# Kernel optimization log

Measured on AMD Instinct MI355X. Metric: run time of the kernel, lower is better.

Reference implementation:

```python
import jax, jax.numpy as jnp
import numpy as np

B, SRC_LEN, IN_DIM = 4096, 128, 16
H = 64
SEQ_LEN = 100
MEAN_DIM = 4
COV_DIM = MEAN_DIM + MEAN_DIM * (MEAN_DIM - 1) // 2  # 10
SKIP = 4


def _lin_init(key, out_d, in_d):
    k1, k2 = jax.random.split(key)
    bound = 1.0 / np.sqrt(in_d)
    W = jax.random.uniform(k1, (out_d, in_d), minval=-bound, maxval=bound, dtype=jnp.float32)
    b = jax.random.uniform(k2, (out_d,), minval=-bound, maxval=bound, dtype=jnp.float32)
    return W, b


def setup_inputs() -> dict:
    key = jax.random.key(0)
    ks = jax.random.split(key, 16)
    inp = {}
    inp["x"] = jax.random.normal(ks[0], (B, SRC_LEN, IN_DIM), dtype=jnp.float32)
    inp["trg"] = jax.random.normal(ks[1], (B, 1, SKIP), dtype=jnp.float32)
    # encoder GRU (1 layer)
    inp["enc_Wih"], inp["enc_bih"] = _lin_init(ks[2], 3 * H, IN_DIM)
    inp["enc_Whh"], inp["enc_bhh"] = _lin_init(ks[3], 3 * H, H)
    # decoder GRU (1 layer)
    inp["dec_Wih"], inp["dec_bih"] = _lin_init(ks[4], 3 * H, IN_DIM)
    inp["dec_Whh"], inp["dec_bhh"] = _lin_init(ks[5], 3 * H, H)
    # decoder.out: Linear(H -> IN_DIM)
    inp["out_W"], inp["out_b"] = _lin_init(ks[6], IN_DIM, H)
    # initEmbed: Linear(SKIP -> IN_DIM)
    inp["emb_W"], inp["emb_b"] = _lin_init(ks[7], IN_DIM, SKIP)
    # mean head: Linear(IN_DIM->H), GELU, Linear(H->MEAN_DIM)
    inp["mh_W1"], inp["mh_b1"] = _lin_init(ks[8], H, IN_DIM)
    inp["mh_W2"], inp["mh_b2"] = _lin_init(ks[9], MEAN_DIM, H)
    # cov head: Linear(IN_DIM->H), GELU, Linear(H->COV_DIM)
    inp["ch_W1"], inp["ch_b1"] = _lin_init(ks[10], H, IN_DIM)
    inp["ch_W2"], inp["ch_b2"] = _lin_init(ks[11], COV_DIM, H)
    return inp


def _gru_cell(h, xt, Wih, Whh, bih, bhh):
    # PyTorch GRU cell math. h, xt: [B, H], [B, in]
    gi = xt @ Wih.T + bih           # [B, 3H]
    gh = h @ Whh.T + bhh            # [B, 3H]
    i_r, i_z, i_n = jnp.split(gi, 3, axis=-1)
    h_r, h_z, h_n = jnp.split(gh, 3, axis=-1)
    r = jax.nn.sigmoid(i_r + h_r)
    z = jax.nn.sigmoid(i_z + h_z)
    n = jnp.tanh(i_n + r * h_n)
    return (1.0 - z) * n + z * h


def reference(x, trg, enc_Wih, enc_bih, enc_Whh, enc_bhh,
              dec_Wih, dec_bih, dec_Whh, dec_bhh,
              out_W, out_b, emb_W, emb_b,
              mh_W1, mh_b1, mh_W2, mh_b2,
              ch_W1, ch_b1, ch_W2, ch_b2):
    b = x.shape[0]
    # ---- encoder GRU over src_len; only final hidden is used downstream ----
    h0 = jnp.zeros((b, H), dtype=x.dtype)

    def enc_step(h, xt):
        h = _gru_cell(h, xt, enc_Wih, enc_Whh, enc_bih, enc_bhh)
        return h, None

    enc_h, _ = jax.lax.scan(enc_step, h0, jnp.swapaxes(x, 0, 1))

    init_in = trg[:, 0, :] @ emb_W.T + emb_b  # [B, IN_DIM]

    def dec_step(carry, _):
        h, inp = carry
        h = _gru_cell(h, inp, dec_Wih, dec_Whh, dec_bih, dec_bhh)
        o = h @ out_W.T + out_b               # [B, IN_DIM]
        nxt = jax.lax.stop_gradient(o)        # .detach() on fed-back input
        return (h, nxt), o

    (_, _), outs = jax.lax.scan(dec_step, (enc_h, init_in), None, length=SEQ_LEN)
    dec_out = jnp.swapaxes(outs, 0, 1)        # [B, SEQ_LEN, IN_DIM]

    # ---- output heads (Dropout is identity in eval) ----
    means = jax.nn.gelu(dec_out @ mh_W1.T + mh_b1, approximate=False) @ mh_W2.T + mh_b2
    covs = jax.nn.gelu(dec_out @ ch_W1.T + ch_b1, approximate=False) @ ch_W2.T + ch_b2

    inf = jnp.inf
    lower = jnp.array([-inf, -inf, -1.0, -1.0], dtype=means.dtype)
    upper = jnp.array([inf, inf, 1.0, 1.0], dtype=means.dtype)
    means = jnp.maximum(jnp.minimum(means, upper), lower)
    return means, covs
```

## Files before the change

kernel.cpp:

```cpp
#include <hip/hip_runtime.h>
#include <cstdint>
#include <cstddef>

#define BTOT    4096
#define SRCLEN  128
#define INDIM   16
#define HDIM    64
#define SEQLEN  100
#define MEANS_N (BTOT * SEQLEN * 4)

__device__ __forceinline__ float sigmoidf_(float x) { return 1.0f / (1.0f + __expf(-x)); }
__device__ __forceinline__ float tanhf_(float x) {
    float e = __expf(2.0f * x);
    return 1.0f - 2.0f / (e + 1.0f);
}
__device__ __forceinline__ float gelu_exact(float x) {
    return 0.5f * x * (1.0f + erff(x * 0.70710678118654752440f));
}

typedef __attribute__((ext_vector_type(8))) short s8v;
typedef __attribute__((ext_vector_type(4))) float f4v;

__device__ __forceinline__ unsigned short f2bf(float x) {
    unsigned u = __float_as_uint(x);
    unsigned r = (u + 0x7FFFu + ((u >> 16) & 1u)) >> 16;
    return (unsigned short)r;
}
__device__ __forceinline__ float bf2f(unsigned short b) {
    return __uint_as_float(((unsigned)b) << 16);
}
__device__ __forceinline__ void split2(float4 a, float4 b, s8v& hi, s8v& lo) {
    float v[8] = {a.x, a.y, a.z, a.w, b.x, b.y, b.z, b.w};
    #pragma unroll
    for (int j = 0; j < 8; ++j) {
        unsigned short h = f2bf(v[j]);
        hi[j] = (short)h;
        lo[j] = (short)f2bf(v[j] - bf2f(h));
    }
}
__device__ __forceinline__ void split8(const float* v, s8v& hi, s8v& lo) {
    #pragma unroll
    for (int j = 0; j < 8; ++j) {
        unsigned short h = f2bf(v[j]);
        hi[j] = (short)h;
        lo[j] = (short)f2bf(v[j] - bf2f(h));
    }
}
__device__ __forceinline__ void load_bfrag(const float* p, s8v& hi, s8v& lo) {
    float4 a = *(const float4*)p;
    float4 b = *(const float4*)(p + 4);
    split2(a, b, hi, lo);
}

#define MFMA16(a, b, c) __builtin_amdgcn_mfma_f32_16x16x32_bf16((a), (b), (c), 0, 0, 0)

__global__ __launch_bounds__(256, 1) void enc_mfma_kernel(
    const float* __restrict__ x,
    const float* __restrict__ Wih, const float* __restrict__ bih,
    const float* __restrict__ Whh, const float* __restrict__ bhh,
    float* __restrict__ enc_h)
{
    const int tid  = threadIdx.x;
    const int lane = tid & 63;
    const int w    = tid >> 6;
    const int col  = lane & 15;
    const int q    = lane >> 4;
    const int u    = w * 16 + col;
    const int b0   = blockIdx.x * 16;

    __shared__ __align__(16) unsigned short hiL[2][16][72];
    __shared__ __align__(16) unsigned short loL[2][16][72];

    for (int i = tid; i < 16 * 72; i += 256) {
        ((unsigned short*)hiL)[i] = 0;
        ((unsigned short*)loL)[i] = 0;
    }

    const s8v z8 = {0, 0, 0, 0, 0, 0, 0, 0};
    const f4v z4 = {0.0f, 0.0f, 0.0f, 0.0f};

    s8v brh[3], brl[3], bzh[3], bzl[3], bnhh[2], bnhl[2], bnxh, bnxl;
    load_bfrag(Whh + (size_t)u * 64 + q * 8,              brh[0], brl[0]);
    load_bfrag(Whh + (size_t)u * 64 + 32 + q * 8,         brh[1], brl[1]);
    load_bfrag(Whh + (size_t)(64 + u) * 64 + q * 8,       bzh[0], bzl[0]);
    load_bfrag(Whh + (size_t)(64 + u) * 64 + 32 + q * 8,  bzh[1], bzl[1]);
    load_bfrag(Whh + (size_t)(128 + u) * 64 + q * 8,      bnhh[0], bnhl[0]);
    load_bfrag(Whh + (size_t)(128 + u) * 64 + 32 + q * 8, bnhh[1], bnhl[1]);
    if (q < 2) {
        load_bfrag(Wih + (size_t)u * 16 + q * 8,         brh[2], brl[2]);
        load_bfrag(Wih + (size_t)(64 + u) * 16 + q * 8,  bzh[2], bzl[2]);
        load_bfrag(Wih + (size_t)(128 + u) * 16 + q * 8, bnxh, bnxl);
    } else {
        brh[2] = z8; brl[2] = z8; bzh[2] = z8; bzl[2] = z8; bnxh = z8; bnxl = z8;
    }

    const float br   = bih[u] + bhh[u];
    const float bz   = bih[u + 64] + bhh[u + 64];
    const float bnx  = bih[u + 128];
    const float bnh  = bhh[u + 128];

    s8v xh = z8, xl = z8;
    if (q < 2) {
        const float* xp = x + ((size_t)(b0 + col) * SRCLEN + 0) * INDIM + q * 8;
        split2(*(const float4*)xp, *(const float4*)(xp + 4), xh, xl);
    }

    f4v hold = z4;
    __syncthreads();

    int cur = 0;
    for (int t = 0; t < SRCLEN; ++t) {
        float4 nx0, nx1;
        const bool pf = (t + 1 < SRCLEN) && (q < 2);
        if (pf) {
            const float* xp = x + ((size_t)(b0 + col) * SRCLEN + (t + 1)) * INDIM + q * 8;
            nx0 = *(const float4*)xp;
            nx1 = *(const float4*)(xp + 4);
        }

        const s8v ah0 = *(const s8v*)&hiL[cur][col][q * 8];
        const s8v al0 = *(const s8v*)&loL[cur][col][q * 8];
        const s8v ah1 = *(const s8v*)&hiL[cur][col][32 + q * 8];
        const s8v al1 = *(const s8v*)&loL[cur][col][32 + q * 8];

        f4v accr, accz, accnh, accnx;
        accr  = MFMA16(ah0, brh[0], z4);
        accz  = MFMA16(ah0, bzh[0], z4);
        accnh = MFMA16(ah0, bnhh[0], z4);
        accr  = MFMA16(ah0, brl[0], accr);
        accz  = MFMA16(ah0, bzl[0], accz);
        accnh = MFMA16(ah0, bnhl[0], accnh);
        accr  = MFMA16(al0, brh[0], accr);
        accz  = MFMA16(al0, bzh[0], accz);
        accnh = MFMA16(al0, bnhh[0], accnh);
        accr  = MFMA16(ah1, brh[1], accr);
        accz  = MFMA16(ah1, bzh[1], accz);
        accnh = MFMA16(ah1, bnhh[1], accnh);
        accr  = MFMA16(ah1, brl[1], accr);
        accz  = MFMA16(ah1, bzl[1], accz);
        accnh = MFMA16(ah1, bnhl[1], accnh);
        accr  = MFMA16(al1, brh[1], accr);
        accz  = MFMA16(al1, bzh[1], accz);
        accnh = MFMA16(al1, bnhh[1], accnh);
        accr  = MFMA16(xh, brh[2], accr);
        accz  = MFMA16(xh, bzh[2], accz);
        accnx = MFMA16(xh, bnxh, z4);
        accr  = MFMA16(xh, brl[2], accr);
        accz  = MFMA16(xh, bzl[2], accz);
        accnx = MFMA16(xh, bnxl, accnx);
        accr  = MFMA16(xl, brh[2], accr);
        accz  = MFMA16(xl, bzh[2], accz);
        accnx = MFMA16(xl, bnxh, accnx);

        const int nxt = cur ^ 1;
        #pragma unroll
        for (int i = 0; i < 4; ++i) {
            float r  = sigmoidf_(accr[i] + br);
            float zz = sigmoidf_(accz[i] + bz);
            float n  = tanhf_(accnx[i] + bnx + r * (accnh[i] + bnh));
            float h  = (1.0f - zz) * n + zz * hold[i];
            hold[i] = h;
            unsigned short hh = f2bf(h);
            hiL[nxt][q * 4 + i][u] = hh;
            loL[nxt][q * 4 + i][u] = f2bf(h - bf2f(hh));
        }
        __syncthreads();

        if (t + 1 < SRCLEN) {
            if (q < 2) split2(nx0, nx1, xh, xl);
        }
        cur ^= 1;
    }

    #pragma unroll
    for (int i = 0; i < 4; ++i)
        enc_h[(size_t)(b0 + q * 4 + i) * HDIM + u] = hold[i];
}

__global__ __launch_bounds__(256, 1) void dec_mfma_kernel(
    const float* __restrict__ trg,
    const float* __restrict__ Wih, const float* __restrict__ bih,
    const float* __restrict__ Whh, const float* __restrict__ bhh,
    const float* __restrict__ outW, const float* __restrict__ outb,
    const float* __restrict__ embW, const float* __restrict__ embb,
    const float* __restrict__ enc_h,
    float* __restrict__ dec_o)
{
    const int tid  = threadIdx.x;
    const int lane = tid & 63;
    const int w    = tid >> 6;
    const int col  = lane & 15;
    const int q    = lane >> 4;
    const int u    = w * 16 + col;
    const int b0   = blockIdx.x * 16;

    __shared__ __align__(16) unsigned short hiL[2][16][72];
    __shared__ __align__(16) unsigned short loL[2][16][72];
    __shared__ float outW_l[16][64];
    __shared__ float init_l[16][16];

    for (int i = tid; i < 16 * 64; i += 256) outW_l[i >> 6][i & 63] = outW[i];
    {
        int b = tid >> 4, jj = tid & 15;
        float s = embb[jj];
        #pragma unroll
        for (int s4 = 0; s4 < 4; ++s4)
            s = fmaf(embW[jj * 4 + s4], trg[(size_t)(b0 + b) * 4 + s4], s);
        init_l[b][jj] = s;
    }
    {
        int idx = tid * 4;
        int bb = idx >> 6, uu = idx & 63;
        float4 v = *(const float4*)(enc_h + (size_t)(b0 + bb) * HDIM + uu);
        float vv[4] = {v.x, v.y, v.z, v.w};
        #pragma unroll
        for (int j = 0; j < 4; ++j) {
            unsigned short hh = f2bf(vv[j]);
            hiL[0][bb][uu + j] = hh;
            loL[0][bb][uu + j] = f2bf(vv[j] - bf2f(hh));
        }
    }
    f4v hold;
    #pragma unroll
    for (int i = 0; i < 4; ++i)
        hold[i] = enc_h[(size_t)(b0 + q * 4 + i) * HDIM + u];

    __syncthreads();

    const f4v z4 = {0.0f, 0.0f, 0.0f, 0.0f};

    float wh_r[16], wh_z[16], wh_n[16];
    #pragma unroll
    for (int c = 0; c < 2; ++c)
        #pragma unroll
        for (int jj = 0; jj < 8; ++jj) {
            int k = c * 32 + q * 8 + jj;
            wh_r[c * 8 + jj] = Whh[(size_t)u * 64 + k];
            wh_z[c * 8 + jj] = Whh[(size_t)(64 + u) * 64 + k];
            wh_n[c * 8 + jj] = Whh[(size_t)(128 + u) * 64 + k];
        }
    float wi_r[16], wi_z[16], wi_n[16];
    #pragma unroll
    for (int j = 0; j < 16; ++j) {
        wi_r[j] = Wih[(size_t)u * 16 + j];
        wi_z[j] = Wih[(size_t)(64 + u) * 16 + j];
        wi_n[j] = Wih[(size_t)(128 + u) * 16 + j];
    }

    float m_r[16], m_z[16], c_in[16];
    #pragma unroll
    for (int c = 0; c < 2; ++c)
        #pragma unroll
        for (int jj = 0; jj < 8; ++jj) {
            int k = c * 32 + q * 8 + jj;
            float sr = 0.0f, sz = 0.0f, sn = 0.0f;
            #pragma unroll
            for (int j = 0; j < 16; ++j) {
                float ow = outW_l[j][k];
                sr = fmaf(wi_r[j], ow, sr);
                sz = fmaf(wi_z[j], ow, sz);
                sn = fmaf(wi_n[j], ow, sn);
            }
            m_r[c * 8 + jj]  = wh_r[c * 8 + jj] + sr;
            m_z[c * 8 + jj]  = wh_z[c * 8 + jj] + sz;
            c_in[c * 8 + jj] = sn;
        }

    s8v mrh[2], mrl[2], mzh[2], mzl[2], cinh[2], cinl[2], hnh[2], hnl[2];
    split8(m_r,      mrh[0],  mrl[0]);  split8(m_r + 8,  mrh[1],  mrl[1]);
    split8(m_z,      mzh[0],  mzl[0]);  split8(m_z + 8,  mzh[1],  mzl[1]);
    split8(c_in,     cinh[0], cinl[0]); split8(c_in + 8, cinh[1], cinl[1]);
    split8(wh_n,     hnh[0],  hnl[0]);  split8(wh_n + 8, hnh[1],  hnl[1]);
    s8v r0h[2], r0l[2], z0h[2], z0l[2];
    split8(wh_r, r0h[0], r0l[0]); split8(wh_r + 8, r0h[1], r0l[1]);
    split8(wh_z, z0h[0], z0l[0]); split8(wh_z + 8, z0h[1], z0l[1]);
    s8v owh[2], owl[2];
    {
        float ov[16];
        #pragma unroll
        for (int c = 0; c < 2; ++c)
            #pragma unroll
            for (int jj = 0; jj < 8; ++jj)
                ov[c * 8 + jj] = outW_l[col][c * 32 + q * 8 + jj];
        split8(ov, owh[0], owl[0]); split8(ov + 8, owh[1], owl[1]);
    }

    float b_r = bhh[u] + bih[u];
    float b_z = bhh[u + 64] + bih[u + 64];
    float b_in = bih[u + 128];
    const float b_hn = bhh[u + 128];
    #pragma unroll
    for (int j = 0; j < 16; ++j) {
        float obj = outb[j];
        b_r  = fmaf(obj, wi_r[j], b_r);
        b_z  = fmaf(obj, wi_z[j], b_z);
        b_in = fmaf(obj, wi_n[j], b_in);
    }
    const float ob = outb[col];

    float g_r[4], g_z[4], g_n[4];
    #pragma unroll
    for (int i = 0; i < 4; ++i) {
        float sr = bih[u] + bhh[u];
        float sz = bih[u + 64] + bhh[u + 64];
        float sn = bih[u + 128];
        #pragma unroll
        for (int j = 0; j < 16; ++j) {
            float iv = init_l[q * 4 + i][j];
            sr = fmaf(wi_r[j], iv, sr);
            sz = fmaf(wi_z[j], iv, sz);
            sn = fmaf(wi_n[j], iv, sn);
        }
        g_r[i] = sr; g_z[i] = sz; g_n[i] = sn;
    }

    {
        const s8v ah0 = *(const s8v*)&hiL[0][col][q * 8];
        const s8v al0 = *(const s8v*)&loL[0][col][q * 8];
        const s8v ah1 = *(const s8v*)&hiL[0][col][32 + q * 8];
        const s8v al1 = *(const s8v*)&loL[0][col][32 + q * 8];
        f4v ar, az, ahn;
        ar  = MFMA16(ah0, r0h[0], z4);
        az  = MFMA16(ah0, z0h[0], z4);
        ahn = MFMA16(ah0, hnh[0], z4);
        ar  = MFMA16(ah0, r0l[0], ar);
        az  = MFMA16(ah0, z0l[0], az);
        ahn = MFMA16(ah0, hnl[0], ahn);
        ar  = MFMA16(al0, r0h[0], ar);
        az  = MFMA16(al0, z0h[0], az);
        ahn = MFMA16(al0, hnh[0], ahn);
        ar  = MFMA16(ah1, r0h[1], ar);
        az  = MFMA16(ah1, z0h[1], az);
        ahn = MFMA16(ah1, hnh[1], ahn);
        ar  = MFMA16(ah1, r0l[1], ar);
        az  = MFMA16(ah1, z0l[1], az);
        ahn = MFMA16(ah1, hnl[1], ahn);
        ar  = MFMA16(al1, r0h[1], ar);
        az  = MFMA16(al1, z0h[1], az);
        ahn = MFMA16(al1, hnh[1], ahn);
        #pragma unroll
        for (int i = 0; i < 4; ++i) {
            float r  = sigmoidf_(ar[i] + g_r[i]);
            float zz = sigmoidf_(az[i] + g_z[i]);
            float n  = tanhf_(g_n[i] + r * (ahn[i] + b_hn));
            float h  = (1.0f - zz) * n + zz * hold[i];
            hold[i] = h;
            unsigned short hh = f2bf(h);
            hiL[1][q * 4 + i][u] = hh;
            loL[1][q * 4 + i][u] = f2bf(h - bf2f(hh));
        }
        __syncthreads();
    }

    for (int t = 1; t < SEQLEN; ++t) {
        const int cur = t & 1;
        const s8v ah0 = *(const s8v*)&hiL[cur][col][q * 8];
        const s8v al0 = *(const s8v*)&loL[cur][col][q * 8];
        const s8v ah1 = *(const s8v*)&hiL[cur][col][32 + q * 8];
        const s8v al1 = *(const s8v*)&loL[cur][col][32 + q * 8];

        if (w == 0) {
            f4v oa;
            oa = MFMA16(ah0, owh[0], z4);
            oa = MFMA16(ah0, owl[0], oa);
            oa = MFMA16(al0, owh[0], oa);
            oa = MFMA16(ah1, owh[1], oa);
            oa = MFMA16(ah1, owl[1], oa);
            oa = MFMA16(al1, owh[1], oa);
            #pragma unroll
            for (int i = 0; i < 4; ++i)
                dec_o[(((size_t)(b0 + q * 4 + i) * SEQLEN) + (t - 1)) * INDIM + col] = oa[i] + ob;
        }

        f4v ar, az, ain, ahn;
        ar  = MFMA16(ah0, mrh[0], z4);
        az  = MFMA16(ah0, mzh[0], z4);
        ain = MFMA16(ah0, cinh[0], z4);
        ahn = MFMA16(ah0, hnh[0], z4);
        ar  = MFMA16(ah0, mrl[0], ar);
        az  = MFMA16(ah0, mzl[0], az);
        ain = MFMA16(ah0, cinl[0], ain);
        ahn = MFMA16(ah0, hnl[0], ahn);
        ar  = MFMA16(al0, mrh[0], ar);
        az  = MFMA16(al0, mzh[0], az);
        ain = MFMA16(al0, cinh[0], ain);
        ahn = MFMA16(al0, hnh[0], ahn);
        ar  = MFMA16(ah1, mrh[1], ar);
        az  = MFMA16(ah1, mzh[1], az);
        ain = MFMA16(ah1, cinh[1], ain);
        ahn = MFMA16(ah1, hnh[1], ahn);
        ar  = MFMA16(ah1, mrl[1], ar);
        az  = MFMA16(ah1, mzl[1], az);
        ain = MFMA16(ah1, cinl[1], ain);
        ahn = MFMA16(ah1, hnl[1], ahn);
        ar  = MFMA16(al1, mrh[1], ar);
        az  = MFMA16(al1, mzh[1], az);
        ain = MFMA16(al1, cinh[1], ain);
        ahn = MFMA16(al1, hnh[1], ahn);

        const int nxt = cur ^ 1;
        #pragma unroll
        for (int i = 0; i < 4; ++i) {
            float r  = sigmoidf_(ar[i] + b_r);
            float zz = sigmoidf_(az[i] + b_z);
            float n  = tanhf_(ain[i] + b_in + r * (ahn[i] + b_hn));
            float h  = (1.0f - zz) * n + zz * hold[i];
            hold[i] = h;
            unsigned short hh = f2bf(h);
            hiL[nxt][q * 4 + i][u] = hh;
            loL[nxt][q * 4 + i][u] = f2bf(h - bf2f(hh));
        }
        __syncthreads();
    }

    if (w == 0) {
        const s8v ah0 = *(const s8v*)&hiL[0][col][q * 8];
        const s8v al0 = *(const s8v*)&loL[0][col][q * 8];
        const s8v ah1 = *(const s8v*)&hiL[0][col][32 + q * 8];
        const s8v al1 = *(const s8v*)&loL[0][col][32 + q * 8];
        f4v oa;
        oa = MFMA16(ah0, owh[0], z4);
        oa = MFMA16(ah0, owl[0], oa);
        oa = MFMA16(al0, owh[0], oa);
        oa = MFMA16(ah1, owh[1], oa);
        oa = MFMA16(ah1, owl[1], oa);
        oa = MFMA16(al1, owh[1], oa);
        #pragma unroll
        for (int i = 0; i < 4; ++i)
            dec_o[(((size_t)(b0 + q * 4 + i) * SEQLEN) + (SEQLEN - 1)) * INDIM + col] = oa[i] + ob;
    }
}

__global__ void heads_kernel(
    const float* __restrict__ dec_o,
    const float* __restrict__ mW1, const float* __restrict__ mb1,
    const float* __restrict__ mW2, const float* __restrict__ mb2,
    const float* __restrict__ cW1, const float* __restrict__ cb1,
    const float* __restrict__ cW2, const float* __restrict__ cb2,
    float* __restrict__ out)
{
    const size_t r = (size_t)blockIdx.x * 256 + threadIdx.x;

    float o16[16];
    {
        const float4* op = (const float4*)(dec_o + r * 16);
        #pragma unroll
        for (int c = 0; c < 4; ++c) {
            float4 v = op[c];
            o16[4 * c + 0] = v.x; o16[4 * c + 1] = v.y;
            o16[4 * c + 2] = v.z; o16[4 * c + 3] = v.w;
        }
    }

    float m[4], cv[10];
    #pragma unroll
    for (int j = 0; j < 4; ++j)  m[j]  = mb2[j];
    #pragma unroll
    for (int j = 0; j < 10; ++j) cv[j] = cb2[j];

    #pragma unroll 8
    for (int hu = 0; hu < 64; ++hu) {
        const float* w1m = mW1 + hu * 16;
        float hm = mb1[hu];
        #pragma unroll
        for (int i = 0; i < 16; ++i) hm = fmaf(w1m[i], o16[i], hm);
        float gm = gelu_exact(hm);
        #pragma unroll
        for (int j = 0; j < 4; ++j) m[j] = fmaf(mW2[j * 64 + hu], gm, m[j]);

        const float* w1c = cW1 + hu * 16;
        float hc = cb1[hu];
        #pragma unroll
        for (int i = 0; i < 16; ++i) hc = fmaf(w1c[i], o16[i], hc);
        float gc = gelu_exact(hc);
        #pragma unroll
        for (int j = 0; j < 10; ++j) cv[j] = fmaf(cW2[j * 64 + hu], gc, cv[j]);
    }

    m[2] = fminf(fmaxf(m[2], -1.0f), 1.0f);
    m[3] = fminf(fmaxf(m[3], -1.0f), 1.0f);

    float* means = out;
    float* covs  = out + MEANS_N;
    #pragma unroll
    for (int j = 0; j < 4; ++j)  means[r * 4 + j]  = m[j];
    #pragma unroll
    for (int j = 0; j < 10; ++j) covs[r * 10 + j]  = cv[j];
}

extern "C" void kernel_launch(void* const* d_in, const int* in_sizes, int n_in,
                              void* d_out, int out_size, void* d_ws, size_t ws_size,
                              hipStream_t stream)
{
    const float* x    = (const float*)d_in[0];
    const float* trg  = (const float*)d_in[1];
    const float* eWih = (const float*)d_in[2];
    const float* ebih = (const float*)d_in[3];
    const float* eWhh = (const float*)d_in[4];
    const float* ebhh = (const float*)d_in[5];
    const float* dWih = (const float*)d_in[6];
    const float* dbih = (const float*)d_in[7];
    const float* dWhh = (const float*)d_in[8];
    const float* dbhh = (const float*)d_in[9];
    const float* outW = (const float*)d_in[10];
    const float* outb = (const float*)d_in[11];
    const float* embW = (const float*)d_in[12];
    const float* embb = (const float*)d_in[13];
    const float* mW1  = (const float*)d_in[14];
    const float* mb1  = (const float*)d_in[15];
    const float* mW2  = (const float*)d_in[16];
    const float* mb2  = (const float*)d_in[17];
    const float* cW1  = (const float*)d_in[18];
    const float* cb1  = (const float*)d_in[19];
    const float* cW2  = (const float*)d_in[20];
    const float* cb2  = (const float*)d_in[21];

    float* ws    = (float*)d_ws;
    float* enc_h = ws;
    float* dec_o = ws + (size_t)BTOT * HDIM;
    float* outp  = (float*)d_out;

    enc_mfma_kernel<<<dim3(BTOT / 16), dim3(256), 0, stream>>>(x, eWih, ebih, eWhh, ebhh, enc_h);
    dec_mfma_kernel<<<dim3(BTOT / 16), dim3(256), 0, stream>>>(trg, dWih, dbih, dWhh, dbhh,
                                                               outW, outb, embW, embb, enc_h, dec_o);
    heads_kernel<<<dim3((BTOT * SEQLEN) / 256), dim3(256), 0, stream>>>(
        dec_o, mW1, mb1, mW2, mb2, cW1, cb1, cW2, cb2, outp);
}
```

Baseline: 430.7 us.

## Halve batch rows per block, stage encoder inputs in LDS, use fast GELU

Encoder and decoder blocks now each process 8 batch rows instead of 16, which doubles the grid to 512 blocks on a latency-bound recurrence. Gate elementwise work is split across lane halves with a cross-lane shuffle so each lane handles 2 rows instead of 4. The encoder pre-stages x, already split into bf16 hi and lo halves, into LDS in two 64-step chunks instead of prefetching per step. Sigmoid, tanh and GELU switch to hardware reciprocal and an erf polynomial approximation, trading a little accuracy for cheaper transcendental math. The MFMA tiles stay 16 rows wide with the upper 8 zero-padded, so half of the MFMA work is wasted.

```diff
diff --git a/kernel.cpp b/kernel.cpp
--- a/kernel.cpp
+++ b/kernel.cpp
@@ -9,13 +9,24 @@
 #define SEQLEN  100
 #define MEANS_N (BTOT * SEQLEN * 4)
 
-__device__ __forceinline__ float sigmoidf_(float x) { return 1.0f / (1.0f + __expf(-x)); }
+__device__ __forceinline__ float sigmoidf_(float x) {
+    return __builtin_amdgcn_rcpf(1.0f + __expf(-x));
+}
 __device__ __forceinline__ float tanhf_(float x) {
     float e = __expf(2.0f * x);
-    return 1.0f - 2.0f / (e + 1.0f);
-}
-__device__ __forceinline__ float gelu_exact(float x) {
-    return 0.5f * x * (1.0f + erff(x * 0.70710678118654752440f));
+    return 1.0f - 2.0f * __builtin_amdgcn_rcpf(e + 1.0f);
+}
+__device__ __forceinline__ float gelu_fast(float x) {
+    float z = fabsf(x) * 0.70710678118654752440f;
+    float t = __builtin_amdgcn_rcpf(1.0f + 0.3275911f * z);
+    float p = t * (0.254829592f +
+              t * (-0.284496736f +
+              t * (1.421413741f +
+              t * (-1.453152027f +
+              t * 1.061405429f))));
+    float er = 1.0f - p * __expf(-z * z);
+    er = copysignf(er, x);
+    return 0.5f * x * (1.0f + er);
 }
 
 typedef __attribute__((ext_vector_type(8))) short s8v;
@@ -52,9 +63,14 @@
     split2(a, b, hi, lo);
 }
 
+__device__ __forceinline__ float half_merge(float own_lo, float send_hi, int lane) {
+    float rec = __shfl_xor(send_hi, 32, 64);
+    return (lane < 32) ? own_lo : rec;
+}
+
 #define MFMA16(a, b, c) __builtin_amdgcn_mfma_f32_16x16x32_bf16((a), (b), (c), 0, 0, 0)
 
-__global__ __launch_bounds__(256, 1) void enc_mfma_kernel(
+__global__ __launch_bounds__(256, 2) void enc_mfma_kernel(
     const float* __restrict__ x,
     const float* __restrict__ Wih, const float* __restrict__ bih,
     const float* __restrict__ Whh, const float* __restrict__ bhh,
@@ -66,15 +82,40 @@
     const int col  = lane & 15;
     const int q    = lane >> 4;
     const int u    = w * 16 + col;
-    const int b0   = blockIdx.x * 16;
+    const int b0   = blockIdx.x * 8;
+    const int rj0  = (q & 1) * 4 + ((q >> 1) << 1);
 
     __shared__ __align__(16) unsigned short hiL[2][16][72];
     __shared__ __align__(16) unsigned short loL[2][16][72];
-
-    for (int i = tid; i < 16 * 72; i += 256) {
+    __shared__ __align__(16) unsigned short xhi_l[64][8][16];
+    __shared__ __align__(16) unsigned short xlo_l[64][8][16];
+
+    for (int i = tid; i < 2 * 16 * 72; i += 256) {
         ((unsigned short*)hiL)[i] = 0;
         ((unsigned short*)loL)[i] = 0;
     }
+
+    auto stage_x = [&](int c) {
+        #pragma unroll
+        for (int k = 0; k < 8; ++k) {
+            int f   = tid + k * 256;
+            int b   = f >> 8;
+            int rem = f & 255;
+            int tl  = rem >> 2;
+            int d4  = (rem & 3) << 2;
+            const float* xp = x + ((size_t)(b0 + b) * SRCLEN + (c * 64 + tl)) * INDIM + d4;
+            float4 v = *(const float4*)xp;
+            float vv[4] = {v.x, v.y, v.z, v.w};
+            unsigned short hh[4], ll[4];
+            #pragma unroll
+            for (int j = 0; j < 4; ++j) {
+                hh[j] = f2bf(vv[j]);
+                ll[j] = f2bf(vv[j] - bf2f(hh[j]));
+            }
+            *(ushort4*)&xhi_l[tl][b][d4] = make_ushort4(hh[0], hh[1], hh[2], hh[3]);
+            *(ushort4*)&xlo_l[tl][b][d4] = make_ushort4(ll[0], ll[1], ll[2], ll[3]);
+        }
+    };
 
     const s8v z8 = {0, 0, 0, 0, 0, 0, 0, 0};
     const f4v z4 = {0.0f, 0.0f, 0.0f, 0.0f};
@@ -99,24 +140,23 @@
     const float bnx  = bih[u + 128];
     const float bnh  = bhh[u + 128];
 
-    s8v xh = z8, xl = z8;
-    if (q < 2) {
-        const float* xp = x + ((size_t)(b0 + col) * SRCLEN + 0) * INDIM + q * 8;
-        split2(*(const float4*)xp, *(const float4*)(xp + 4), xh, xl);
-    }
-
-    f4v hold = z4;
+    stage_x(0);
+    float hold2[2] = {0.0f, 0.0f};
     __syncthreads();
 
     int cur = 0;
     for (int t = 0; t < SRCLEN; ++t) {
-        float4 nx0, nx1;
-        const bool pf = (t + 1 < SRCLEN) && (q < 2);
-        if (pf) {
-            const float* xp = x + ((size_t)(b0 + col) * SRCLEN + (t + 1)) * INDIM + q * 8;
-            nx0 = *(const float4*)xp;
-            nx1 = *(const float4*)(xp + 4);
-        }
+        if (t == 64) {
+            stage_x(1);
+            __syncthreads();
+        }
+        const int tl = t & 63;
+
+        s8v xh, xl;
+        if (q < 2 && col < 8) {
+            xh = *(const s8v*)&xhi_l[tl][col][q * 8];
+            xl = *(const s8v*)&xlo_l[tl][col][q * 8];
+        } else { xh = z8; xl = z8; }
 
         const s8v ah0 = *(const s8v*)&hiL[cur][col][q * 8];
         const s8v al0 = *(const s8v*)&loL[cur][col][q * 8];
@@ -152,32 +192,37 @@
         accz  = MFMA16(xl, bzh[2], accz);
         accnx = MFMA16(xl, bnxh, accnx);
 
+        float pr[2], pz[2], pnh[2], pnx[2];
+        pr[0]  = half_merge(accr[0],  accr[2],  lane);
+        pr[1]  = half_merge(accr[1],  accr[3],  lane);
+        pz[0]  = half_merge(accz[0],  accz[2],  lane);
+        pz[1]  = half_merge(accz[1],  accz[3],  lane);
+        pnh[0] = half_merge(accnh[0], accnh[2], lane);
+        pnh[1] = half_merge(accnh[1], accnh[3], lane);
+        pnx[0] = half_merge(accnx[0], accnx[2], lane);
+        pnx[1] = half_merge(accnx[1], accnx[3], lane);
+
         const int nxt = cur ^ 1;
         #pragma unroll
-        for (int i = 0; i < 4; ++i) {
-            float r  = sigmoidf_(accr[i] + br);
-            float zz = sigmoidf_(accz[i] + bz);
-            float n  = tanhf_(accnx[i] + bnx + r * (accnh[i] + bnh));
-            float h  = (1.0f - zz) * n + zz * hold[i];
-            hold[i] = h;
+        for (int j = 0; j < 2; ++j) {
+            float r  = sigmoidf_(pr[j] + br);
+            float zz = sigmoidf_(pz[j] + bz);
+            float n  = tanhf_(pnx[j] + bnx + r * (pnh[j] + bnh));
+            float h  = (1.0f - zz) * n + zz * hold2[j];
+            hold2[j] = h;
             unsigned short hh = f2bf(h);
-            hiL[nxt][q * 4 + i][u] = hh;
-            loL[nxt][q * 4 + i][u] = f2bf(h - bf2f(hh));
+            hiL[nxt][rj0 + j][u] = hh;
+            loL[nxt][rj0 + j][u] = f2bf(h - bf2f(hh));
         }
         __syncthreads();
-
-        if (t + 1 < SRCLEN) {
-            if (q < 2) split2(nx0, nx1, xh, xl);
-        }
         cur ^= 1;
     }
 
-    #pragma unroll
-    for (int i = 0; i < 4; ++i)
-        enc_h[(size_t)(b0 + q * 4 + i) * HDIM + u] = hold[i];
-}
-
-__global__ __launch_bounds__(256, 1) void dec_mfma_kernel(
+    enc_h[(size_t)(b0 + rj0) * HDIM + u]     = hold2[0];
+    enc_h[(size_t)(b0 + rj0 + 1) * HDIM + u] = hold2[1];
+}
+
+__global__ __launch_bounds__(256, 2) void dec_mfma_kernel(
     const float* __restrict__ trg,
     const float* __restrict__ Wih, const float* __restrict__ bih,
     const float* __restrict__ Whh, const float* __restrict__ bhh,
@@ -192,15 +237,16 @@
     const int col  = lane & 15;
     const int q    = lane >> 4;
     const int u    = w * 16 + col;
-    const int b0   = blockIdx.x * 16;
+    const int b0   = blockIdx.x * 8;
+    const int rj0  = (q & 1) * 4 + ((q >> 1) << 1);
 
     __shared__ __align__(16) unsigned short hiL[2][16][72];
     __shared__ __align__(16) unsigned short loL[2][16][72];
     __shared__ float outW_l[16][64];
-    __shared__ float init_l[16][16];
+    __shared__ float init_l[8][16];
 
     for (int i = tid; i < 16 * 64; i += 256) outW_l[i >> 6][i & 63] = outW[i];
-    {
+    if (tid < 128) {
         int b = tid >> 4, jj = tid & 15;
         float s = embb[jj];
         #pragma unroll
@@ -208,7 +254,14 @@
             s = fmaf(embW[jj * 4 + s4], trg[(size_t)(b0 + b) * 4 + s4], s);
         init_l[b][jj] = s;
     }
-    {
+    for (int i = tid; i < 2 * 8 * 72; i += 256) {
+        int buf = i / (8 * 72);
+        int rr  = (i / 72) & 7;
+        int cc  = i % 72;
+        hiL[buf][8 + rr][cc] = 0;
+        loL[buf][8 + rr][cc] = 0;
+    }
+    if (tid < 128) {
         int idx = tid * 4;
         int bb = idx >> 6, uu = idx & 63;
         float4 v = *(const float4*)(enc_h + (size_t)(b0 + bb) * HDIM + uu);
@@ -220,10 +273,9 @@
             loL[0][bb][uu + j] = f2bf(vv[j] - bf2f(hh));
         }
     }
-    f4v hold;
-    #pragma unroll
-    for (int i = 0; i < 4; ++i)
-        hold[i] = enc_h[(size_t)(b0 + q * 4 + i) * HDIM + u];
+    float hold2[2];
+    hold2[0] = enc_h[(size_t)(b0 + rj0) * HDIM + u];
+    hold2[1] = enc_h[(size_t)(b0 + rj0 + 1) * HDIM + u];
 
     __syncthreads();
 
@@ -298,20 +350,21 @@
     }
     const float ob = outb[col];
 
-    float g_r[4], g_z[4], g_n[4];
-    #pragma unroll
-    for (int i = 0; i < 4; ++i) {
+    float g_r[2], g_z[2], g_n[2];
+    #pragma unroll
+    for (int j2 = 0; j2 < 2; ++j2) {
+        int row = rj0 + j2;
         float sr = bih[u] + bhh[u];
         float sz = bih[u + 64] + bhh[u + 64];
         float sn = bih[u + 128];
         #pragma unroll
         for (int j = 0; j < 16; ++j) {
-            float iv = init_l[q * 4 + i][j];
+            float iv = init_l[row][j];
             sr = fmaf(wi_r[j], iv, sr);
             sz = fmaf(wi_z[j], iv, sz);
             sn = fmaf(wi_n[j], iv, sn);
         }
-        g_r[i] = sr; g_z[i] = sz; g_n[i] = sn;
+        g_r[j2] = sr; g_z[j2] = sz; g_n[j2] = sn;
     }
 
     {
@@ -338,16 +391,25 @@
         ar  = MFMA16(al1, r0h[1], ar);
         az  = MFMA16(al1, z0h[1], az);
         ahn = MFMA16(al1, hnh[1], ahn);
-        #pragma unroll
-        for (int i = 0; i < 4; ++i) {
-            float r  = sigmoidf_(ar[i] + g_r[i]);
-            float zz = sigmoidf_(az[i] + g_z[i]);
-            float n  = tanhf_(g_n[i] + r * (ahn[i] + b_hn));
-            float h  = (1.0f - zz) * n + zz * hold[i];
-            hold[i] = h;
+
+        float pr[2], pz[2], pnh[2];
+        pr[0]  = half_merge(ar[0],  ar[2],  lane);
+        pr[1]  = half_merge(ar[1],  ar[3],  lane);
+        pz[0]  = half_merge(az[0],  az[2],  lane);
+        pz[1]  = half_merge(az[1],  az[3],  lane);
+        pnh[0] = half_merge(ahn[0], ahn[2], lane);
+        pnh[1] = half_merge(ahn[1], ahn[3], lane);
+
+        #pragma unroll
+        for (int j = 0; j < 2; ++j) {
+            float r  = sigmoidf_(pr[j] + g_r[j]);
+            float zz = sigmoidf_(pz[j] + g_z[j]);
+            float n  = tanhf_(g_n[j] + r * (pnh[j] + b_hn));
+            float h  = (1.0f - zz) * n + zz * hold2[j];
+            hold2[j] = h;
             unsigned short hh = f2bf(h);
-            hiL[1][q * 4 + i][u] = hh;
-            loL[1][q * 4 + i][u] = f2bf(h - bf2f(hh));
+            hiL[1][rj0 + j][u] = hh;
+            loL[1][rj0 + j][u] = f2bf(h - bf2f(hh));
         }
         __syncthreads();
     }
@@ -367,9 +429,11 @@
             oa = MFMA16(ah1, owh[1], oa);
             oa = MFMA16(ah1, owl[1], oa);
             oa = MFMA16(al1, owh[1], oa);
-            #pragma unroll
-            for (int i = 0; i < 4; ++i)
-                dec_o[(((size_t)(b0 + q * 4 + i) * SEQLEN) + (t - 1)) * INDIM + col] = oa[i] + ob;
+            if (q < 2) {
+                #pragma unroll
+                for (int i = 0; i < 4; ++i)
+                    dec_o[(((size_t)(b0 + q * 4 + i) * SEQLEN) + (t - 1)) * INDIM + col] = oa[i] + ob;
+            }
         }
 
         f4v ar, az, ain, ahn;
@@ -398,17 +462,27 @@
         ain = MFMA16(al1, cinh[1], ain);
         ahn = MFMA16(al1, hnh[1], ahn);
 
+        float pr[2], pz[2], pin[2], pnh[2];
+        pr[0]  = half_merge(ar[0],  ar[2],  lane);
+        pr[1]  = half_merge(ar[1],  ar[3],  lane);
+        pz[0]  = half_merge(az[0],  az[2],  lane);
+        pz[1]  = half_merge(az[1],  az[3],  lane);
+        pin[0] = half_merge(ain[0], ain[2], lane);
+        pin[1] = half_merge(ain[1], ain[3], lane);
+        pnh[0] = half_merge(ahn[0], ahn[2], lane);
+        pnh[1] = half_merge(ahn[1], ahn[3], lane);
+
         const int nxt = cur ^ 1;
         #pragma unroll
-        for (int i = 0; i < 4; ++i) {
-            float r  = sigmoidf_(ar[i] + b_r);
-            float zz = sigmoidf_(az[i] + b_z);
-            float n  = tanhf_(ain[i] + b_in + r * (ahn[i] + b_hn));
-            float h  = (1.0f - zz) * n + zz * hold[i];
-            hold[i] = h;
+        for (int j = 0; j < 2; ++j) {
+            float r  = sigmoidf_(pr[j] + b_r);
+            float zz = sigmoidf_(pz[j] + b_z);
+            float n  = tanhf_(pin[j] + b_in + r * (pnh[j] + b_hn));
+            float h  = (1.0f - zz) * n + zz * hold2[j];
+            hold2[j] = h;
             unsigned short hh = f2bf(h);
-            hiL[nxt][q * 4 + i][u] = hh;
-            loL[nxt][q * 4 + i][u] = f2bf(h - bf2f(hh));
+            hiL[nxt][rj0 + j][u] = hh;
+            loL[nxt][rj0 + j][u] = f2bf(h - bf2f(hh));
         }
         __syncthreads();
     }
@@ -425,9 +499,11 @@
         oa = MFMA16(ah1, owh[1], oa);
         oa = MFMA16(ah1, owl[1], oa);
         oa = MFMA16(al1, owh[1], oa);
-        #pragma unroll
-        for (int i = 0; i < 4; ++i)
-            dec_o[(((size_t)(b0 + q * 4 + i) * SEQLEN) + (SEQLEN - 1)) * INDIM + col] = oa[i] + ob;
+        if (q < 2) {
+            #pragma unroll
+            for (int i = 0; i < 4; ++i)
+                dec_o[(((size_t)(b0 + q * 4 + i) * SEQLEN) + (SEQLEN - 1)) * INDIM + col] = oa[i] + ob;
+        }
     }
 }
 
@@ -464,7 +540,7 @@
         float hm = mb1[hu];
         #pragma unroll
         for (int i = 0; i < 16; ++i) hm = fmaf(w1m[i], o16[i], hm);
-        float gm = gelu_exact(hm);
+        float gm = gelu_fast(hm);
         #pragma unroll
         for (int j = 0; j < 4; ++j) m[j] = fmaf(mW2[j * 64 + hu], gm, m[j]);
 
@@ -472,7 +548,7 @@
         float hc = cb1[hu];
         #pragma unroll
         for (int i = 0; i < 16; ++i) hc = fmaf(w1c[i], o16[i], hc);
-        float gc = gelu_exact(hc);
+        float gc = gelu_fast(hc);
         #pragma unroll
         for (int j = 0; j < 10; ++j) cv[j] = fmaf(cW2[j * 64 + hu], gc, cv[j]);
     }
@@ -520,9 +596,9 @@
     float* dec_o = ws + (size_t)BTOT * HDIM;
     float* outp  = (float*)d_out;
 
-    enc_mfma_kernel<<<dim3(BTOT / 16), dim3(256), 0, stream>>>(x, eWih, ebih, eWhh, ebhh, enc_h);
-    dec_mfma_kernel<<<dim3(BTOT / 16), dim3(256), 0, stream>>>(trg, dWih, dbih, dWhh, dbhh,
-                                                               outW, outb, embW, embb, enc_h, dec_o);
+    enc_mfma_kernel<<<dim3(BTOT / 8), dim3(256), 0, stream>>>(x, eWih, ebih, eWhh, ebhh, enc_h);
+    dec_mfma_kernel<<<dim3(BTOT / 8), dim3(256), 0, stream>>>(trg, dWih, dbih, dWhh, dbhh,
+                                                              outW, outb, embW, embb, enc_h, dec_o);
     heads_kernel<<<dim3((BTOT * SEQLEN) / 256), dim3(256), 0, stream>>>(
         dec_o, mW1, mb1, mW2, mb2, cW1, cb1, cW2, cb2, outp);
 }
```

After: 388.3 us. 9.8% less time.
